# Kernel optimization log

Measured on AMD Instinct MI355X. Metric: run time of the kernel, lower is better.

Reference implementation:

```python
import jax, jax.numpy as jnp
import numpy as np

B, T, H, OUT_STEPS, D = 131072, 51, 64, 20, 4


def setup_inputs() -> dict:
    key = jax.random.key(0)
    ks = jax.random.split(key, 11)
    s = 1.0 / np.sqrt(H)  # torch nn.GRU / nn.Linear uniform init bound
    u = lambda k, shape: jax.random.uniform(k, shape, jnp.float32, -s, s)
    return {
        "input_seq": jax.random.normal(ks[0], (B, T, D), jnp.float32),
        "enc_Wih": u(ks[1], (3 * H, D)),
        "enc_Whh": u(ks[2], (3 * H, H)),
        "enc_bih": u(ks[3], (3 * H,)),
        "enc_bhh": u(ks[4], (3 * H,)),
        "dec_Wih": u(ks[5], (3 * H, D)),
        "dec_Whh": u(ks[6], (3 * H, H)),
        "dec_bih": u(ks[7], (3 * H,)),
        "dec_bhh": u(ks[8], (3 * H,)),
        "lin_W": u(ks[9], (D, H)),
        "lin_b": u(ks[10], (D,)),
    }


def _gru_cell(x, h, Wih, Whh, bih, bhh):
    """PyTorch GRU cell semantics. x: [B,D_in], h: [B,H]."""
    gi = x @ Wih.T + bih  # [B,3H]
    gh = h @ Whh.T + bhh  # [B,3H]
    ir, iz, inn = jnp.split(gi, 3, axis=-1)
    hr, hz, hn = jnp.split(gh, 3, axis=-1)
    r = jax.nn.sigmoid(ir + hr)
    z = jax.nn.sigmoid(iz + hz)
    n = jnp.tanh(inn + r * hn)
    return (1.0 - z) * n + z * h


def reference(input_seq, enc_Wih, enc_Whh, enc_bih, enc_bhh,
              dec_Wih, dec_Whh, dec_bih, dec_bhh, lin_W, lin_b):
    # offset: last observed point, broadcast over the 20 output steps
    offset = input_seq[:, -1:, :]  # [B,1,D]
    diffs = input_seq[:, 1:] - input_seq[:, :-1]  # [B,T-1,D]; dropout p=0 -> identity
    h0 = jnp.zeros((input_seq.shape[0], H), input_seq.dtype)

    def enc_step(h, x_t):
        return _gru_cell(x_t, h, enc_Wih, enc_Whh, enc_bih, enc_bhh), None

    hn, _ = jax.lax.scan(enc_step, h0, jnp.swapaxes(diffs, 0, 1))  # final hidden [B,H]

    def dec_step(carry, _):
        h, px = carry
        h = _gru_cell(px, h, dec_Wih, dec_Whh, dec_bih, dec_bhh)
        x = h @ lin_W.T + lin_b + px  # linear + residual
        return (h, x), x

    _, xs = jax.lax.scan(dec_step, (hn, diffs[:, -1]), None, length=OUT_STEPS)
    out = jnp.swapaxes(xs, 0, 1)  # [B,OUT_STEPS,D]
    return out + offset
```

## Files before the change

### kernel.cpp

```cpp
#include <hip/hip_runtime.h>

namespace {

constexpr int kT = 51;
constexpr int kOut = 20;
constexpr float kL2E  = 1.4426950408889634f;
constexpr float kL2E2 = 2.8853900817779268f;

typedef __attribute__((ext_vector_type(8))) short bf16x8;
typedef __attribute__((ext_vector_type(4))) float f32x4;
typedef __attribute__((ext_vector_type(2))) float f32x2;

union FragU {
    bf16x8 v;
    unsigned long long u64[2];
    unsigned int u32[4];
    unsigned short s[8];
};

__device__ __forceinline__ unsigned short f2bf(float x) {
    union { float f; unsigned int u; } v;
    v.f = x;
    unsigned int r = (v.u + 0x7fffu + ((v.u >> 16) & 1u)) >> 16;
    return (unsigned short)r;
}

__device__ __forceinline__ unsigned int cvtpk(float a, float b) {
    unsigned int r;
    asm("v_cvt_pk_bf16_f32 %0, %1, %2" : "=v"(r) : "v"(a), "v"(b));
    return r;
}

__global__ __launch_bounds__(256, 2) void gru_encdec(
    const float* __restrict__ input,
    const float* __restrict__ eWih, const float* __restrict__ eWhh,
    const float* __restrict__ ebih, const float* __restrict__ ebhh,
    const float* __restrict__ dWih, const float* __restrict__ dWhh,
    const float* __restrict__ dbih, const float* __restrict__ dbhh,
    const float* __restrict__ linW, const float* __restrict__ linb,
    float* __restrict__ out)
{
    __shared__ __align__(16) unsigned short hbuf[2][4][16 * 68];

    const int lane = (int)(threadIdx.x & 63u);
    const int w = (int)(threadIdx.x >> 6u);
    const int q = lane >> 4;
    const int i = lane & 15;
    const bool q0 = (q == 0);
    const long bb = (long)blockIdx.x * 64 + i;

    const float* xrow[4];
#pragma unroll
    for (int g = 0; g < 4; ++g) xrow[g] = input + (bb + 16 * g) * (kT * 4);

    bf16x8 WA[3][2];
    bf16x8 WAUG[3];
    f32x4 bhhn4;
    float hp[4][4];
    bf16x8 bh[4][2];
    float px[4][4];
    const f32x4 z4 = {0.f, 0.f, 0.f, 0.f};
    const bf16x8 zfr = {0, 0, 0, 0, 0, 0, 0, 0};

    auto load_whh = [&](const float* __restrict__ Whh) {
#pragma unroll
        for (int l = 0; l < 3; ++l) {
            const int tau = 4 * l + w;
            const float sc = (l < 2) ? kL2E : kL2E2;
#pragma unroll
            for (int f = 0; f < 2; ++f) {
                const float* ptr = Whh + (tau * 16 + i) * 64 + f * 32 + q * 8;
                FragU fu;
#pragma unroll
                for (int j = 0; j < 8; ++j) fu.s[j] = f2bf(ptr[j] * sc);
                WA[l][f] = fu.v;
            }
        }
    };

    auto load_aug = [&](const float* __restrict__ Wih,
                        const float* __restrict__ bih,
                        const float* __restrict__ bhh) {
#pragma unroll
        for (int l = 0; l < 3; ++l) {
            const int tau = 4 * l + w;
            const float sc = (l < 2) ? kL2E : kL2E2;
            FragU fu;
            fu.u64[0] = 0; fu.u64[1] = 0;
            if (q0) {
                int j = tau * 16 + i;
#pragma unroll
                for (int d = 0; d < 4; ++d) fu.s[d] = f2bf(Wih[j * 4 + d] * sc);
                float bias = (l < 2) ? (bih[j] + bhh[j]) : bih[j];
                fu.s[4] = f2bf(bias * sc);
            }
            WAUG[l] = fu.v;
        }
#pragma unroll
        for (int r = 0; r < 4; ++r)
            bhhn4[r] = bhh[128 + 16 * w + 4 * q + r] * kL2E2;
    };

    auto make_baug = [&](const float* pxv) -> bf16x8 {
        FragU fu;
        fu.u32[0] = cvtpk(pxv[0], pxv[1]);
        fu.u32[1] = cvtpk(pxv[2], pxv[3]);
        fu.u32[2] = 0x3f80u;
        fu.u32[3] = 0u;
        return fu.v;
    };

    auto gru_step = [&](int ssel, const bf16x8* ba) {
#pragma unroll
        for (int p = 0; p < 2; ++p) {
            const int g0 = 2 * p, g1 = 2 * p + 1;
            f32x4 R[2], Z[2], Ni[2], Nh[2];
#pragma unroll
            for (int k = 0; k < 2; ++k) {
                const int g = 2 * p + k;
                R[k] = __builtin_amdgcn_mfma_f32_16x16x32_bf16(WAUG[0], ba[g], z4, 0, 0, 0);
                R[k] = __builtin_amdgcn_mfma_f32_16x16x32_bf16(WA[0][0], bh[g][0], R[k], 0, 0, 0);
                R[k] = __builtin_amdgcn_mfma_f32_16x16x32_bf16(WA[0][1], bh[g][1], R[k], 0, 0, 0);
                Z[k] = __builtin_amdgcn_mfma_f32_16x16x32_bf16(WAUG[1], ba[g], z4, 0, 0, 0);
                Z[k] = __builtin_amdgcn_mfma_f32_16x16x32_bf16(WA[1][0], bh[g][0], Z[k], 0, 0, 0);
                Z[k] = __builtin_amdgcn_mfma_f32_16x16x32_bf16(WA[1][1], bh[g][1], Z[k], 0, 0, 0);
                Ni[k] = __builtin_amdgcn_mfma_f32_16x16x32_bf16(WAUG[2], ba[g], z4, 0, 0, 0);
                Nh[k] = __builtin_amdgcn_mfma_f32_16x16x32_bf16(WA[2][0], bh[g][0], bhhn4, 0, 0, 0);
                Nh[k] = __builtin_amdgcn_mfma_f32_16x16x32_bf16(WA[2][1], bh[g][1], Nh[k], 0, 0, 0);
            }
            float hva[4], hvb[4];
            const f32x2 one = {1.f, 1.f};
            const f32x2 m2 = {-2.f, -2.f};
#pragma unroll
            for (int r = 0; r < 4; ++r) {
                f32x2 a = { __builtin_amdgcn_exp2f(-R[0][r]),
                            __builtin_amdgcn_exp2f(-R[1][r]) };
                f32x2 c = { __builtin_amdgcn_exp2f(-Z[0][r]),
                            __builtin_amdgcn_exp2f(-Z[1][r]) };
                f32x2 A = a + one, C = c + one;
                f32x2 P = A * C;
                float rpp = __builtin_amdgcn_rcpf(P.x * P.y);
                f32x2 Ps = {P.y, P.x};
                f32x2 rp = rpp * Ps;
                f32x2 rr = rp * C;
                f32x2 zz = rp * A;
                f32x2 Nh2 = {Nh[0][r], Nh[1][r]};
                f32x2 Ni2 = {Ni[0][r], Ni[1][r]};
                f32x2 p2 = __builtin_elementwise_fma(rr, Nh2, Ni2);
                f32x2 E = { __builtin_amdgcn_exp2f(p2.x),
                            __builtin_amdgcn_exp2f(p2.y) };
                f32x2 D = E + one;
                float rdd = __builtin_amdgcn_rcpf(D.x * D.y);
                f32x2 Ds = {D.y, D.x};
                f32x2 t = rdd * Ds;
                f32x2 n = __builtin_elementwise_fma(t, m2, one);
                f32x2 h = {hp[g0][r], hp[g1][r]};
                f32x2 hv = __builtin_elementwise_fma(zz, h - n, n);
                hp[g0][r] = hv.x; hp[g1][r] = hv.y;
                hva[r] = hv.x;    hvb[r] = hv.y;
            }
            uint2 wva, wvb;
            wva.x = cvtpk(hva[0], hva[1]); wva.y = cvtpk(hva[2], hva[3]);
            wvb.x = cvtpk(hvb[0], hvb[1]); wvb.y = cvtpk(hvb[2], hvb[3]);
            *(uint2*)&hbuf[ssel][g0][i * 68 + 16 * w + 4 * q] = wva;
            *(uint2*)&hbuf[ssel][g1][i * 68 + 16 * w + 4 * q] = wvb;
        }
        __syncthreads();
#pragma unroll
        for (int g = 0; g < 4; ++g) {
            const unsigned short* hw = hbuf[ssel][g];
            FragU fA, fB;
            fA.u64[0] = *(const unsigned long long*)&hw[i * 68 + 8 * q];
            fA.u64[1] = *(const unsigned long long*)&hw[i * 68 + 8 * q + 4];
            fB.u64[0] = *(const unsigned long long*)&hw[i * 68 + 32 + 8 * q];
            fB.u64[1] = *(const unsigned long long*)&hw[i * 68 + 32 + 8 * q + 4];
            bh[g][0] = fA.v;
            bh[g][1] = fB.v;
        }
    };

#pragma unroll
    for (int g = 0; g < 4; ++g) {
#pragma unroll
        for (int r = 0; r < 4; ++r) hp[g][r] = 0.f;
        bh[g][0] = zfr;
        bh[g][1] = zfr;
    }
    load_whh(eWhh);
    load_aug(eWih, ebih, ebhh);

    float4 xp[4], xn[4];
#pragma unroll
    for (int g = 0; g < 4; ++g) {
        xp[g] = *(const float4*)(xrow[g]);
        xn[g] = *(const float4*)(xrow[g] + 4);
    }
    bf16x8 ba[4];
#pragma unroll 2
    for (int s = 0; s < kT - 1; ++s) {
#pragma unroll
        for (int g = 0; g < 4; ++g) {
            px[g][0] = xn[g].x - xp[g].x; px[g][1] = xn[g].y - xp[g].y;
            px[g][2] = xn[g].z - xp[g].z; px[g][3] = xn[g].w - xp[g].w;
            xp[g] = xn[g];
        }
        int idx = s + 2; if (idx > kT - 1) idx = kT - 1;
#pragma unroll
        for (int g = 0; g < 4; ++g)
            xn[g] = *(const float4*)(xrow[g] + idx * 4);
#pragma unroll
        for (int g = 0; g < 4; ++g) ba[g] = make_baug(px[g]);
        gru_step(s & 1, ba);
    }
    float4 off[4];
#pragma unroll
    for (int g = 0; g < 4; ++g) off[g] = xp[g];

    load_whh(dWhh);
    load_aug(dWih, dbih, dbhh);

    bf16x8 AL0, AL1;
    {
        FragU a0, a1;
        a0.u64[0] = a0.u64[1] = 0;
        a1.u64[0] = a1.u64[1] = 0;
        if (i < 4) {
            const float* p0 = linW + i * 64 + q * 8;
            const float* p1 = linW + i * 64 + 32 + q * 8;
#pragma unroll
            for (int j = 0; j < 8; ++j) {
                a0.s[j] = f2bf(p0[j]);
                a1.s[j] = f2bf(p1[j]);
            }
        }
        AL0 = a0.v; AL1 = a1.v;
    }
    const float lb0 = linb[0], lb1 = linb[1], lb2 = linb[2], lb3 = linb[3];

#pragma unroll 2
    for (int s = 0; s < kOut; ++s) {
#pragma unroll
        for (int g = 0; g < 4; ++g) ba[g] = make_baug(px[g]);
        gru_step(s & 1, ba);
#pragma unroll
        for (int g = 0; g < 4; ++g) {
            f32x4 X = __builtin_amdgcn_mfma_f32_16x16x32_bf16(AL0, bh[g][0], z4, 0, 0, 0);
            X = __builtin_amdgcn_mfma_f32_16x16x32_bf16(AL1, bh[g][1], X, 0, 0, 0);
            px[g][0] += X[0] + lb0; px[g][1] += X[1] + lb1;
            px[g][2] += X[2] + lb2; px[g][3] += X[3] + lb3;
        }
#pragma unroll
        for (int g = 0; g < 4; ++g) {
            if (w == g && q0) {
                float* op = out + (bb + 16 * g) * (kOut * 4) + s * 4;
                float4 v;
                v.x = px[g][0] + off[g].x; v.y = px[g][1] + off[g].y;
                v.z = px[g][2] + off[g].z; v.w = px[g][3] + off[g].w;
                *(float4*)op = v;
            }
        }
    }
}

}

extern "C" void kernel_launch(void* const* d_in, const int* in_sizes, int n_in,
                              void* d_out, int out_size, void* d_ws, size_t ws_size,
                              hipStream_t stream) {
    const float* input = (const float*)d_in[0];
    const float* eWih = (const float*)d_in[1];
    const float* eWhh = (const float*)d_in[2];
    const float* ebih = (const float*)d_in[3];
    const float* ebhh = (const float*)d_in[4];
    const float* dWih = (const float*)d_in[5];
    const float* dWhh = (const float*)d_in[6];
    const float* dbih = (const float*)d_in[7];
    const float* dbhh = (const float*)d_in[8];
    const float* linW = (const float*)d_in[9];
    const float* linb = (const float*)d_in[10];
    float* out = (float*)d_out;

    const int B = in_sizes[0] / (kT * 4);
    const int nblocks = B / 64;
    gru_encdec<<<nblocks, 256, 0, stream>>>(input, eWih, eWhh, ebih, ebhh,
                                            dWih, dWhh, dbih, dbhh,
                                            linW, linb, out);
}
```

Before: 648.6 us.

## Raise occupancy to three blocks per CU by trimming register-resident input state

Raises launch bounds from 2 to 3 blocks per multiprocessor and cuts live registers to make that fit. The per-group B-augment fragments are now built inside the GRU step right before use, and the double-buffered input prefetch (xp/xn) collapses to one current-row register set that also serves as the final offset. The aim is more resident waves to hide MFMA and transcendental latency. In exchange the next-timestep input load is no longer prefetched a step ahead, so global-load latency is exposed in the serial recurrence, and the tighter register budget may cause spills.

Result: slower. 691.7 us (+6.6%).

```diff
diff --git a/kernel.cpp b/kernel.cpp
--- a/kernel.cpp
+++ b/kernel.cpp
@@ -31,7 +31,7 @@
     return r;
 }
 
-__global__ __launch_bounds__(256, 2) void gru_encdec(
+__global__ __launch_bounds__(256, 3) void gru_encdec(
     const float* __restrict__ input,
     const float* __restrict__ eWih, const float* __restrict__ eWhh,
     const float* __restrict__ ebih, const float* __restrict__ ebhh,
@@ -110,7 +110,7 @@
         return fu.v;
     };
 
-    auto gru_step = [&](int ssel, const bf16x8* ba) {
+    auto gru_step = [&](int ssel) {
 #pragma unroll
         for (int p = 0; p < 2; ++p) {
             const int g0 = 2 * p, g1 = 2 * p + 1;
@@ -118,13 +118,14 @@
 #pragma unroll
             for (int k = 0; k < 2; ++k) {
                 const int g = 2 * p + k;
-                R[k] = __builtin_amdgcn_mfma_f32_16x16x32_bf16(WAUG[0], ba[g], z4, 0, 0, 0);
+                const bf16x8 ba = make_baug(px[g]);
+                R[k] = __builtin_amdgcn_mfma_f32_16x16x32_bf16(WAUG[0], ba, z4, 0, 0, 0);
                 R[k] = __builtin_amdgcn_mfma_f32_16x16x32_bf16(WA[0][0], bh[g][0], R[k], 0, 0, 0);
                 R[k] = __builtin_amdgcn_mfma_f32_16x16x32_bf16(WA[0][1], bh[g][1], R[k], 0, 0, 0);
-                Z[k] = __builtin_amdgcn_mfma_f32_16x16x32_bf16(WAUG[1], ba[g], z4, 0, 0, 0);
+                Z[k] = __builtin_amdgcn_mfma_f32_16x16x32_bf16(WAUG[1], ba, z4, 0, 0, 0);
                 Z[k] = __builtin_amdgcn_mfma_f32_16x16x32_bf16(WA[1][0], bh[g][0], Z[k], 0, 0, 0);
                 Z[k] = __builtin_amdgcn_mfma_f32_16x16x32_bf16(WA[1][1], bh[g][1], Z[k], 0, 0, 0);
-                Ni[k] = __builtin_amdgcn_mfma_f32_16x16x32_bf16(WAUG[2], ba[g], z4, 0, 0, 0);
+                Ni[k] = __builtin_amdgcn_mfma_f32_16x16x32_bf16(WAUG[2], ba, z4, 0, 0, 0);
                 Nh[k] = __builtin_amdgcn_mfma_f32_16x16x32_bf16(WA[2][0], bh[g][0], bhhn4, 0, 0, 0);
                 Nh[k] = __builtin_amdgcn_mfma_f32_16x16x32_bf16(WA[2][1], bh[g][1], Nh[k], 0, 0, 0);
             }
@@ -189,32 +190,20 @@
     load_whh(eWhh);
     load_aug(eWih, ebih, ebhh);
 
-    float4 xp[4], xn[4];
-#pragma unroll
-    for (int g = 0; g < 4; ++g) {
-        xp[g] = *(const float4*)(xrow[g]);
-        xn[g] = *(const float4*)(xrow[g] + 4);
-    }
-    bf16x8 ba[4];
+    float4 xc[4];
+#pragma unroll
+    for (int g = 0; g < 4; ++g) xc[g] = *(const float4*)(xrow[g]);
 #pragma unroll 2
     for (int s = 0; s < kT - 1; ++s) {
 #pragma unroll
         for (int g = 0; g < 4; ++g) {
-            px[g][0] = xn[g].x - xp[g].x; px[g][1] = xn[g].y - xp[g].y;
-            px[g][2] = xn[g].z - xp[g].z; px[g][3] = xn[g].w - xp[g].w;
-            xp[g] = xn[g];
-        }
-        int idx = s + 2; if (idx > kT - 1) idx = kT - 1;
-#pragma unroll
-        for (int g = 0; g < 4; ++g)
-            xn[g] = *(const float4*)(xrow[g] + idx * 4);
-#pragma unroll
-        for (int g = 0; g < 4; ++g) ba[g] = make_baug(px[g]);
-        gru_step(s & 1, ba);
-    }
-    float4 off[4];
-#pragma unroll
-    for (int g = 0; g < 4; ++g) off[g] = xp[g];
+            float4 xn = *(const float4*)(xrow[g] + (s + 1) * 4);
+            px[g][0] = xn.x - xc[g].x; px[g][1] = xn.y - xc[g].y;
+            px[g][2] = xn.z - xc[g].z; px[g][3] = xn.w - xc[g].w;
+            xc[g] = xn;
+        }
+        gru_step(s & 1);
+    }
 
     load_whh(dWhh);
     load_aug(dWih, dbih, dbhh);
@@ -239,9 +228,7 @@
 
 #pragma unroll 2
     for (int s = 0; s < kOut; ++s) {
-#pragma unroll
-        for (int g = 0; g < 4; ++g) ba[g] = make_baug(px[g]);
-        gru_step(s & 1, ba);
+        gru_step(s & 1);
 #pragma unroll
         for (int g = 0; g < 4; ++g) {
             f32x4 X = __builtin_amdgcn_mfma_f32_16x16x32_bf16(AL0, bh[g][0], z4, 0, 0, 0);
@@ -254,8 +241,8 @@
             if (w == g && q0) {
                 float* op = out + (bb + 16 * g) * (kOut * 4) + s * 4;
                 float4 v;
-                v.x = px[g][0] + off[g].x; v.y = px[g][1] + off[g].y;
-                v.z = px[g][2] + off[g].z; v.w = px[g][3] + off[g].w;
+                v.x = px[g][0] + xc[g].x; v.y = px[g][1] + xc[g].y;
+                v.z = px[g][2] + xc[g].z; v.w = px[g][3] + xc[g].w;
                 *(float4*)op = v;
             }
         }
```
